# Performance work log

Hardware: AMD Instinct MI355X
Metric: run time of the kernel (lower is better)

The kernel has to match this reference:

```python
import jax, jax.numpy as jnp
import numpy as np

N_HEADS = 16


def _rope(x, cos, sin):
    # x: (B,H,S,hd); cos,sin: (1,1,S,hd//2). Full-dim rotation (rot_dim == head_dim).
    xe = x[..., 0::2]
    xo = x[..., 1::2]
    re = xe * cos - xo * sin
    ro = xe * sin + xo * cos
    return jnp.stack([re, ro], axis=-1).reshape(x.shape)


def setup_inputs() -> dict:
    key = jax.random.key(0)
    B, S, D = 2, 2048, 1024
    hd = D // N_HEADS
    k1, k2, k3, k4, k5 = jax.random.split(key, 5)
    x = jax.random.normal(k1, (B, S, D), dtype=jnp.float32)
    # Linear params (lecun-normal-ish scale)
    w_qkv = jax.random.normal(k2, (D, 3 * D), dtype=jnp.float32) / np.sqrt(D)
    b_qkv = jnp.zeros((3 * D,), dtype=jnp.float32)
    w_out = jax.random.normal(k3, (D, D), dtype=jnp.float32) / np.sqrt(D)
    b_out = jnp.zeros((D,), dtype=jnp.float32)
    # Rotary tables: (S, hd//2)
    inv_freq = 1.0 / (10000.0 ** (np.arange(0, hd, 2, dtype=np.float32) / hd))
    angles = jnp.asarray(np.arange(S, dtype=np.float32)[:, None] * inv_freq[None, :])
    cos = jnp.cos(angles)
    sin = jnp.sin(angles)
    # Causal mask (seq, seq), True = attend
    mask = jnp.tril(jnp.ones((S, S), dtype=bool))
    return {"x": x, "w_qkv": w_qkv, "b_qkv": b_qkv, "w_out": w_out,
            "b_out": b_out, "cos": cos, "sin": sin, "mask": mask}


def reference(x, w_qkv, b_qkv, w_out, b_out, cos, sin, mask):
    B, S, D = x.shape
    H = N_HEADS
    hd = D // H
    scale = hd ** (-0.5)
    qkv = x @ w_qkv + b_qkv  # (B,S,3D)
    qkv = qkv.reshape(B, S, 3, H, hd).transpose(2, 0, 3, 1, 4)  # (3,B,H,S,hd)
    q, k, v = qkv[0], qkv[1], qkv[2]
    c = cos[None, None, :, :]
    s = sin[None, None, :, :]
    q = _rope(q, c, s)
    k = _rope(k, c, s)
    attn = jnp.einsum('bhqd,bhkd->bhqk', q, k) * scale
    attn = jnp.where(mask, attn, -1e9)
    attn = jax.nn.softmax(attn, axis=-1)
    out = jnp.einsum('bhqk,bhkd->bhqd', attn, v)
    out = out.transpose(0, 2, 1, 3).reshape(B, S, D)
    return out @ w_out + b_out
```

## Files before the change

kernel.cpp:

```cpp
#include <hip/hip_runtime.h>
#include <stdint.h>

typedef unsigned short u16;
typedef __attribute__((ext_vector_type(8))) __bf16 bf16x8;
typedef __attribute__((ext_vector_type(4))) float f32x4;
typedef __attribute__((ext_vector_type(4))) unsigned short u16x4;

__device__ __forceinline__ float bf2f(u16 u){
  unsigned int x = ((unsigned int)u) << 16;
  return __builtin_bit_cast(float, x);
}
__device__ __forceinline__ u16 f2bf(float f){
  return __builtin_bit_cast(u16, (__bf16)f);
}
__device__ __forceinline__ float fexp2(float x){ return __builtin_exp2f(x); }
__device__ __forceinline__ void lds_load16(const void* g, void* l){
  __builtin_amdgcn_global_load_lds(
      (const __attribute__((address_space(1))) unsigned int*)g,
      (__attribute__((address_space(3))) unsigned int*)l, 16, 0, 0);
}

__global__ __launch_bounds__(256) void transpose64(const float* __restrict__ in,
                                                   u16* __restrict__ out,
                                                   int R, int C){
  __shared__ u16 t[64][65];
  const int c0 = blockIdx.x * 64, r0 = blockIdx.y * 64;
  const int tid = threadIdx.x;
  const int rr = tid >> 3;
  const int cc = (tid & 7) * 8;
#pragma unroll
  for (int i = 0; i < 2; i++){
    int r = i * 32 + rr;
    const float* p = in + (size_t)(r0 + r) * C + c0 + cc;
    f32x4 v0 = *(const f32x4*)p;
    f32x4 v1 = *(const f32x4*)(p + 4);
#pragma unroll
    for (int j = 0; j < 4; j++){ t[r][cc + j] = f2bf(v0[j]); t[r][cc + 4 + j] = f2bf(v1[j]); }
  }
  __syncthreads();
#pragma unroll
  for (int i = 0; i < 2; i++){
    int c = i * 32 + rr;
    u16 tmp[8];
#pragma unroll
    for (int j = 0; j < 8; j++) tmp[j] = t[cc + j][c];
    *(bf16x8*)(out + (size_t)(c0 + c) * R + r0 + cc) = *(const bf16x8*)tmp;
  }
}

__global__ __launch_bounds__(256) void convert_bf16(const float* __restrict__ in,
                                                    u16* __restrict__ out){
  int t = blockIdx.x * 256 + threadIdx.x;
  const float* p = in + (size_t)t * 8;
  f32x4 v0 = *(const f32x4*)p;
  f32x4 v1 = *(const f32x4*)(p + 4);
  u16 tmp[8];
#pragma unroll
  for (int j = 0; j < 4; j++){ tmp[j] = f2bf(v0[j]); tmp[4 + j] = f2bf(v1[j]); }
  *(bf16x8*)(out + (size_t)t * 8) = *(const bf16x8*)tmp;
}

__global__ __launch_bounds__(256) void v_transpose(const u16* __restrict__ qkv,
                                                   u16* __restrict__ vT){
  const int S = 2048, LD = 3072;
  __shared__ u16 t[64][65];
  const int bh = blockIdx.y;
  const int b = bh >> 4, h = bh & 15;
  const int s0 = blockIdx.x * 64;
  const u16* src = qkv + (size_t)b * S * LD + 2048 + h * 64;
  const int tid = threadIdx.x;
  const int rr = tid >> 3;
  const int cc = (tid & 7) * 8;
#pragma unroll
  for (int i = 0; i < 2; i++){
    int s = i * 32 + rr;
    bf16x8 v = *(const bf16x8*)(src + (size_t)(s0 + s) * LD + cc);
#pragma unroll
    for (int j = 0; j < 8; j++) t[s][cc + j] = __builtin_bit_cast(u16, (__bf16)v[j]);
  }
  __syncthreads();
  u16* dst = vT + (size_t)bh * 64 * S;
#pragma unroll
  for (int i = 0; i < 2; i++){
    int d = i * 32 + rr;
    u16 tmp[8];
#pragma unroll
    for (int j = 0; j < 8; j++) tmp[j] = t[cc + j][d];
    *(bf16x8*)(dst + (size_t)d * S + s0 + cc) = *(const bf16x8*)tmp;
  }
}

template<bool OUTF32, bool ROPE>
__global__ __launch_bounds__(256, 2) void gemm_bt(const u16* __restrict__ A,
                                                  const u16* __restrict__ Bt,
                                                  const float* __restrict__ bias,
                                                  void* __restrict__ Cv,
                                                  int M, int N, int K,
                                                  const float* __restrict__ cosb,
                                                  const float* __restrict__ sinb){
  __shared__ u16 As[128 * 32];
  __shared__ u16 Bs[128 * 32];
  const int nx = gridDim.x;
  const int L = blockIdx.x + nx * blockIdx.y;
  const int per = (nx * gridDim.y) >> 3;
  const int wg = (L & 7) * per + (L >> 3);
  const int bn = wg % nx, bm = wg / nx;
  const int tid = threadIdx.x, w = tid >> 6, l = tid & 63;
  const int lo = l & 15, hi = l >> 4;
  const int wr = (w >> 1) * 64, wc = (w & 1) * 64;
  f32x4 acc[4][4] = {};
  const int lrow = l >> 2, lcd = l & 3;

  for (int k0 = 0; k0 < K; k0 += 32){
#pragma unroll
    for (int i = 0; i < 2; i++){
      int row0 = i * 64 + w * 16;
      int row = row0 + lrow;
      int cs = lcd ^ ((row >> 1) & 3);
      lds_load16(A  + (size_t)(bm * 128 + row) * K + k0 + cs * 8,
                 (char*)As + row0 * 64);
      lds_load16(Bt + (size_t)(bn * 128 + row) * K + k0 + cs * 8,
                 (char*)Bs + row0 * 64);
    }
    __syncthreads();
    bf16x8 a[4], b[4];
#pragma unroll
    for (int mi = 0; mi < 4; mi++){
      int row = wr + mi * 16 + lo;
      unsigned byte = (unsigned)(row * 64 + hi * 16) ^ (((row >> 1) & 3) << 4);
      a[mi] = *(const bf16x8*)((const char*)As + byte);
    }
#pragma unroll
    for (int ni = 0; ni < 4; ni++){
      int row = wc + ni * 16 + lo;
      unsigned byte = (unsigned)(row * 64 + hi * 16) ^ (((row >> 1) & 3) << 4);
      b[ni] = *(const bf16x8*)((const char*)Bs + byte);
    }
    __builtin_amdgcn_s_setprio(1);
#pragma unroll
    for (int mi = 0; mi < 4; mi++)
#pragma unroll
      for (int ni = 0; ni < 4; ni++)
        acc[mi][ni] = __builtin_amdgcn_mfma_f32_16x16x32_bf16(a[mi], b[ni], acc[mi][ni], 0, 0, 0);
    __builtin_amdgcn_s_setprio(0);
    __syncthreads();
  }
  if (ROPE && bn < 16){
#pragma unroll
    for (int mi = 0; mi < 4; mi++){
#pragma unroll
      for (int r = 0; r < 4; r++){
        int grow = bm * 128 + wr + mi * 16 + hi * 4 + r;
        int stok = grow & 2047;
#pragma unroll
        for (int ni = 0; ni < 4; ni++){
          int col = bn * 128 + wc + ni * 16 + lo;
          float v = acc[mi][ni][r] + bias[col];
          float partner = __shfl_xor(v, 1, 64);
          int ip = (col & 63) >> 1;
          float c = cosb[stok * 32 + ip], sn = sinb[stok * 32 + ip];
          float res = (lo & 1) ? (partner * sn + v * c) : (v * c - partner * sn);
          ((u16*)Cv)[(size_t)grow * N + col] = f2bf(res);
        }
      }
    }
  } else {
#pragma unroll
    for (int mi = 0; mi < 4; mi++){
#pragma unroll
      for (int r = 0; r < 4; r++){
        int grow = bm * 128 + wr + mi * 16 + hi * 4 + r;
#pragma unroll
        for (int ni = 0; ni < 4; ni++){
          int col = bn * 128 + wc + ni * 16 + lo;
          float v = acc[mi][ni][r] + bias[col];
          if (OUTF32)
            ((float*)Cv)[(size_t)grow * N + col] = v;
          else
            ((u16*)Cv)[(size_t)grow * N + col] = f2bf(v);
        }
      }
    }
  }
}

#define FA_PHASE(T_, OA_, OB_, MA_, MB_, LA_, LB_)                             \
  {                                                                            \
    const int q0p = (T_) * 32;                                                 \
    const int qrA = q0p + lo, qrB = q0p + 16 + lo;                             \
    const int nkt = (T_) + 1;                                                  \
    const int ch = (nkt + 1) >> 1;                                             \
    const int k0 = w ? ch : 0;                                                 \
    const int k1 = w ? nkt : ch;                                               \
    bf16x8 qfA0, qfA1, qfB0, qfB1;                                             \
    {                                                                          \
      bf16x8 va0 = *(const bf16x8*)(Qp + (size_t)qrA * LD + hi * 8);           \
      bf16x8 va1 = *(const bf16x8*)(Qp + (size_t)qrA * LD + 32 + hi * 8);      \
      bf16x8 vb0 = *(const bf16x8*)(Qp + (size_t)qrB * LD + hi * 8);           \
      bf16x8 vb1 = *(const bf16x8*)(Qp + (size_t)qrB * LD + 32 + hi * 8);      \
      _Pragma("unroll")                                                        \
      for (int j = 0; j < 8; j++){                                             \
        qfA0[j] = (__bf16)((float)va0[j] * QSC);                               \
        qfA1[j] = (__bf16)((float)va1[j] * QSC);                               \
        qfB0[j] = (__bf16)((float)vb0[j] * QSC);                               \
        qfB1[j] = (__bf16)((float)vb1[j] * QSC);                               \
      }                                                                        \
    }                                                                          \
    float lparA = 0.f, lparB = 0.f;                                            \
    MA_ = -1e30f; MB_ = -1e30f;                                                \
    if (k0 < k1){                                                              \
      _Pragma("unroll")                                                        \
      for (int i = 0; i < 4; i++)                                              \
        lds_load16(Kp + (size_t)(k0 * 32 + i * 8 + srow8) * LD + scs * 8,      \
                   (char*)&Ks[w][0][0] + i * 1024);                            \
    }                                                                          \
    int cur = 0;                                                               \
    for (int kt = k0; kt < k1; kt++){                                          \
      bf16x8 vb[4];                                                            \
      _Pragma("unroll")                                                        \
      for (int fd = 0; fd < 4; fd++)                                           \
        vb[fd] = *(const bf16x8*)(Vb + (size_t)(fd * 16 + lo) * S +            \
                                  kt * 32 + hi * 8);                           \
      bf16x8 kb[2][2];                                                         \
      _Pragma("unroll")                                                        \
      for (int c = 0; c < 2; c++){                                             \
        _Pragma("unroll")                                                      \
        for (int f = 0; f < 2; f++){                                           \
          int srw = f * 16 + lo;                                               \
          unsigned byte = ((unsigned)(srw * 128 + c * 64 + hi * 16)) ^         \
                          ((lo & 7) << 4);                                     \
          kb[c][f] = *(const bf16x8*)((const char*)&Ks[w][cur][0] + byte);     \
        }                                                                      \
      }                                                                        \
      if (kt + 1 < k1){                                                        \
        _Pragma("unroll")                                                      \
        for (int i = 0; i < 4; i++)                                            \
          lds_load16(Kp + (size_t)((kt + 1) * 32 + i * 8 + srow8) * LD +       \
                         scs * 8,                                              \
                     (char*)&Ks[w][cur ^ 1][0] + i * 1024);                    \
      }                                                                        \
      f32x4 saA[2] = {}, saB[2] = {};                                          \
      __builtin_amdgcn_s_setprio(1);                                           \
      _Pragma("unroll")                                                        \
      for (int f = 0; f < 2; f++){                                             \
        saA[f] = __builtin_amdgcn_mfma_f32_16x16x32_bf16(kb[0][f], qfA0,       \
                                                         saA[f], 0, 0, 0);     \
        saB[f] = __builtin_amdgcn_mfma_f32_16x16x32_bf16(kb[0][f], qfB0,       \
                                                         saB[f], 0, 0, 0);     \
        saA[f] = __builtin_amdgcn_mfma_f32_16x16x32_bf16(kb[1][f], qfA1,       \
                                                         saA[f], 0, 0, 0);     \
        saB[f] = __builtin_amdgcn_mfma_f32_16x16x32_bf16(kb[1][f], qfB1,       \
                                                         saB[f], 0, 0, 0);     \
      }                                                                        \
      __builtin_amdgcn_s_setprio(0);                                           \
      if (kt == nkt - 1){                                                      \
        _Pragma("unroll")                                                      \
        for (int f = 0; f < 2; f++){                                           \
          int key0 = kt * 32 + f * 16 + hi * 4;                                \
          _Pragma("unroll")                                                    \
          for (int r = 0; r < 4; r++){                                         \
            if (key0 + r > qrA) saA[f][r] = -1e30f;                            \
            if (key0 + r > qrB) saB[f][r] = -1e30f;                            \
          }                                                                    \
        }                                                                      \
      }                                                                        \
      float pmA = fmaxf(                                                       \
          fmaxf(fmaxf(saA[0][0], saA[0][1]), fmaxf(saA[0][2], saA[0][3])),     \
          fmaxf(fmaxf(saA[1][0], saA[1][1]), fmaxf(saA[1][2], saA[1][3])));    \
      float pmB = fmaxf(                                                       \
          fmaxf(fmaxf(saB[0][0], saB[0][1]), fmaxf(saB[0][2], saB[0][3])),     \
          fmaxf(fmaxf(saB[1][0], saB[1][1]), fmaxf(saB[1][2], saB[1][3])));    \
      if (!__all(fmaxf(pmA - MA_, pmB - MB_) <= 11.5f)){                       \
        float rmA = fmaxf(pmA, __shfl_xor(pmA, 16, 64));                       \
        rmA = fmaxf(rmA, __shfl_xor(rmA, 32, 64));                             \
        float rmB = fmaxf(pmB, __shfl_xor(pmB, 16, 64));                       \
        rmB = fmaxf(rmB, __shfl_xor(rmB, 32, 64));                             \
        float mnA = fmaxf(MA_, rmA), mnB = fmaxf(MB_, rmB);                    \
        float cA = fexp2(MA_ - mnA), cB = fexp2(MB_ - mnB);                    \
        MA_ = mnA; MB_ = mnB;                                                  \
        lparA *= cA; lparB *= cB;                                              \
        float cqA[4], cqB[4];                                                  \
        _Pragma("unroll")                                                      \
        for (int r = 0; r < 4; r++){                                           \
          cqA[r] = __shfl(cA, hi * 4 + r, 64);                                 \
          cqB[r] = __shfl(cB, hi * 4 + r, 64);                                 \
        }                                                                      \
        _Pragma("unroll")                                                      \
        for (int fd = 0; fd < 4; fd++){                                        \
          _Pragma("unroll")                                                    \
          for (int r = 0; r < 4; r++){                                         \
            OA_[fd][r] *= cqA[r]; OB_[fd][r] *= cqB[r];                        \
          }                                                                    \
        }                                                                      \
      }                                                                        \
      float pvA[2][4], pvB[2][4];                                              \
      _Pragma("unroll")                                                        \
      for (int f = 0; f < 2; f++){                                             \
        _Pragma("unroll")                                                      \
        for (int r = 0; r < 4; r++){                                           \
          pvA[f][r] = fexp2(saA[f][r] - MA_);                                  \
          pvB[f][r] = fexp2(saB[f][r] - MB_);                                  \
        }                                                                      \
      }                                                                        \
      _Pragma("unroll")                                                        \
      for (int f = 0; f < 2; f++){                                             \
        u16x4 pkA, pkB;                                                        \
        _Pragma("unroll")                                                      \
        for (int r = 0; r < 4; r++){                                           \
          pkA[r] = f2bf(pvA[f][r]); pkB[r] = f2bf(pvB[f][r]);                  \
        }                                                                      \
        *(u16x4*)((char*)&Ps[w][0][0] + lo * 72 + f * 32 + hi * 8) = pkA;      \
        *(u16x4*)((char*)&Ps[w][1][0] + lo * 72 + f * 32 + hi * 8) = pkB;      \
      }                                                                        \
      lparA += ((pvA[0][0] + pvA[0][1]) + (pvA[0][2] + pvA[0][3]))             \
             + ((pvA[1][0] + pvA[1][1]) + (pvA[1][2] + pvA[1][3]));            \
      lparB += ((pvB[0][0] + pvB[0][1]) + (pvB[0][2] + pvB[0][3]))             \
             + ((pvB[1][0] + pvB[1][1]) + (pvB[1][2] + pvB[1][3]));            \
      bf16x8 paA = *(const bf16x8*)((const char*)&Ps[w][0][0] + lo * 72 +      \
                                    hi * 16);                                  \
      bf16x8 paB = *(const bf16x8*)((const char*)&Ps[w][1][0] + lo * 72 +      \
                                    hi * 16);                                  \
      __builtin_amdgcn_s_setprio(1);                                           \
      _Pragma("unroll")                                                        \
      for (int fd = 0; fd < 4; fd++){                                          \
        OA_[fd] = __builtin_amdgcn_mfma_f32_16x16x32_bf16(paA, vb[fd],         \
                                                          OA_[fd], 0, 0, 0);   \
        OB_[fd] = __builtin_amdgcn_mfma_f32_16x16x32_bf16(paB, vb[fd],         \
                                                          OB_[fd], 0, 0, 0);   \
      }                                                                        \
      __builtin_amdgcn_s_setprio(0);                                           \
      cur ^= 1;                                                                \
    }                                                                          \
    lparA += __shfl_xor(lparA, 16, 64); lparA += __shfl_xor(lparA, 32, 64);    \
    lparB += __shfl_xor(lparB, 16, 64); lparB += __shfl_xor(lparB, 32, 64);    \
    LA_ = lparA; LB_ = lparB;                                                  \
  }

#define FA_WRITEPART(slot_, OA_, OB_, MA_, MB_, LA_, LB_)                      \
  {                                                                            \
    _Pragma("unroll")                                                          \
    for (int fd = 0; fd < 4; fd++){                                            \
      u16x4 pkA, pkB;                                                          \
      _Pragma("unroll")                                                        \
      for (int r = 0; r < 4; r++){                                             \
        pkA[r] = f2bf(OA_[fd][r]); pkB[r] = f2bf(OB_[fd][r]);                  \
      }                                                                        \
      *(u16x4*)((char*)&Xo[slot_][0] + (fd * 16 + lo) * 64 + hi * 8) = pkA;    \
      *(u16x4*)((char*)&Xo[slot_][0] + (fd * 16 + lo) * 64 + 32 + hi * 8) = pkB;\
    }                                                                          \
    if (hi == 0){                                                              \
      Xm[slot_][lo] = MA_;      Xl[slot_][lo] = LA_;                           \
      Xm[slot_][16 + lo] = MB_; Xl[slot_][16 + lo] = LB_;                      \
    }                                                                          \
  }

#define FA_COMBINE(slot_, T_, OA_, OB_, MA_, MB_, LA_, LB_)                    \
  {                                                                            \
    const int q0p = (T_) * 32;                                                 \
    u16x4 pA[4], pB[4];                                                        \
    _Pragma("unroll")                                                          \
    for (int fd = 0; fd < 4; fd++){                                            \
      pA[fd] = *(const u16x4*)((const char*)&Xo[slot_][0] +                    \
                               (fd * 16 + lo) * 64 + hi * 8);                  \
      pB[fd] = *(const u16x4*)((const char*)&Xo[slot_][0] +                    \
                               (fd * 16 + lo) * 64 + 32 + hi * 8);             \
    }                                                                          \
    _Pragma("unroll")                                                          \
    for (int r = 0; r < 4; r++){                                               \
      float mOA = __shfl(MA_, hi * 4 + r, 64);                                 \
      float lOA = __shfl(LA_, hi * 4 + r, 64);                                 \
      float mOB = __shfl(MB_, hi * 4 + r, 64);                                 \
      float lOB = __shfl(LB_, hi * 4 + r, 64);                                 \
      float mPA = Xm[slot_][hi * 4 + r], lPA = Xl[slot_][hi * 4 + r];          \
      float mPB = Xm[slot_][16 + hi * 4 + r], lPB = Xl[slot_][16 + hi * 4 + r];\
      float MfA = fmaxf(mOA, mPA), MfB = fmaxf(mOB, mPB);                      \
      float c0A = fexp2(mOA - MfA), c1A = fexp2(mPA - MfA);                    \
      float c0B = fexp2(mOB - MfB), c1B = fexp2(mPB - MfB);                    \
      float invA = 1.0f / (lOA * c0A + lPA * c1A);                             \
      float invB = 1.0f / (lOB * c0B + lPB * c1B);                             \
      int srA = q0p + hi * 4 + r;                                              \
      int srB = q0p + 16 + hi * 4 + r;                                         \
      u16* orA = Oout + (size_t)(b * S + srA) * 1024 + h * 64;                 \
      u16* orB = Oout + (size_t)(b * S + srB) * 1024 + h * 64;                 \
      _Pragma("unroll")                                                        \
      for (int fd = 0; fd < 4; fd++){                                          \
        float vA = (OA_[fd][r] * c0A + bf2f(pA[fd][r]) * c1A) * invA;          \
        float vB = (OB_[fd][r] * c0B + bf2f(pB[fd][r]) * c1B) * invB;          \
        orA[fd * 16 + lo] = f2bf(vA);                                          \
        orB[fd * 16 + lo] = f2bf(vB);                                          \
      }                                                                        \
    }                                                                          \
  }

__global__ __launch_bounds__(128, 2) void flash_attn(const u16* __restrict__ qkv,
                                                     const u16* __restrict__ vT,
                                                     u16* __restrict__ Oout){
  const int S = 2048, LD = 3072;
  const int L = blockIdx.x;
  const int bh = L & 31;
  const int bx = L >> 5;
  const int b = bh >> 4, h = bh & 15;
  const u16* base = qkv + (size_t)b * S * LD;
  const u16* Qp = base + h * 64;
  const u16* Kp = base + 1024 + h * 64;
  const u16* Vb = vT + (size_t)bh * 64 * S;
  const int tid = threadIdx.x, w = tid >> 6, l = tid & 63;
  const int lo = l & 15, hi = l >> 4;
  __shared__ u16 Ks[2][2][32 * 64];
  __shared__ u16 Ps[2][2][16 * 36];
  __shared__ u16 Xo[2][32 * 64];
  __shared__ float Xm[2][32], Xl[2][32];

  const float QSC = 0.125f * 1.44269504089f;
  const int srow8 = l >> 3;
  const int scs = (l & 7) ^ srow8;

  f32x4 o1A[4] = {}, o1B[4] = {};
  f32x4 o2A[4] = {}, o2B[4] = {};
  float m1A, m1B, l1A, l1B, m2A, m2B, l2A, l2B;

  FA_PHASE(63 - bx, o1A, o1B, m1A, m1B, l1A, l1B);
  if (w == 1) FA_WRITEPART(0, o1A, o1B, m1A, m1B, l1A, l1B);
  FA_PHASE(bx,      o2A, o2B, m2A, m2B, l2A, l2B);
  if (w == 0) FA_WRITEPART(1, o2A, o2B, m2A, m2B, l2A, l2B);
  __syncthreads();
  if (w == 0){
    FA_COMBINE(0, 63 - bx, o1A, o1B, m1A, m1B, l1A, l1B);
  } else {
    FA_COMBINE(1, bx,      o2A, o2B, m2A, m2B, l2A, l2B);
  }
}

extern "C" void kernel_launch(void* const* d_in, const int* in_sizes, int n_in,
                              void* d_out, int out_size, void* d_ws, size_t ws_size,
                              hipStream_t stream){
  const float* x     = (const float*)d_in[0];
  const float* w_qkv = (const float*)d_in[1];
  const float* b_qkv = (const float*)d_in[2];
  const float* w_out = (const float*)d_in[3];
  const float* b_out = (const float*)d_in[4];
  const float* cosb  = (const float*)d_in[5];
  const float* sinb  = (const float*)d_in[6];
  float* out = (float*)d_out;
  char* ws = (char*)d_ws;
  u16* qkv  = (u16*)(ws);
  u16* attn = (u16*)(ws + 25165824);
  u16* xbf  = attn;
  u16* wT2  = (u16*)(ws + 33554432);
  u16* wT1  = (u16*)(ws + 35651584);
  u16* vT   = (u16*)(ws + 35651584);

  transpose64<<<dim3(48, 16), 256, 0, stream>>>(w_qkv, wT1, 1024, 3072);
  transpose64<<<dim3(16, 16), 256, 0, stream>>>(w_out, wT2, 1024, 1024);
  convert_bf16<<<2048, 256, 0, stream>>>(x, xbf);
  gemm_bt<false, true ><<<dim3(24, 32), 256, 0, stream>>>(xbf, wT1, b_qkv, qkv,
                                                          4096, 3072, 1024, cosb, sinb);
  v_transpose<<<dim3(32, 32), 256, 0, stream>>>(qkv, vT);
  flash_attn<<<1024, 128, 0, stream>>>(qkv, vT, attn);
  gemm_bt<true , false><<<dim3(8, 32), 256, 0, stream>>>(attn, wT2, b_out, out,
                                                         4096, 1024, 1024, cosb, sinb);
}
```

Before: 129.6 us.

## Merge prep kernels, pad attention combine LDS, raise GEMM occupancy hint

Merges the two weight transposes and the x bf16 conversion into a single prep kernel dispatched by block index, removing two kernel launches and letting the three jobs run concurrently. Pads the flash-attention partial-output LDS rows from 64 to 72 bytes to cut bank conflicts in the cross-wave combine. Raises the GEMM launch-bounds min-blocks hint from 2 to 3, which may force register spills in exchange for higher occupancy.

Measured after the change: 129.3 us. Within noise of the previous version (-0.2%).

```diff
diff --git a/kernel.cpp b/kernel.cpp
--- a/kernel.cpp
+++ b/kernel.cpp
@@ -20,11 +20,11 @@
       (__attribute__((address_space(3))) unsigned int*)l, 16, 0, 0);
 }
 
-__global__ __launch_bounds__(256) void transpose64(const float* __restrict__ in,
-                                                   u16* __restrict__ out,
-                                                   int R, int C){
-  __shared__ u16 t[64][65];
-  const int c0 = blockIdx.x * 64, r0 = blockIdx.y * 64;
+__device__ __forceinline__ void transpose_body(const float* __restrict__ in,
+                                               u16* __restrict__ out,
+                                               int R, int C, int bx, int by,
+                                               u16 (*t)[65]){
+  const int c0 = bx * 64, r0 = by * 64;
   const int tid = threadIdx.x;
   const int rr = tid >> 3;
   const int cc = (tid & 7) * 8;
@@ -48,16 +48,30 @@
   }
 }
 
-__global__ __launch_bounds__(256) void convert_bf16(const float* __restrict__ in,
-                                                    u16* __restrict__ out){
-  int t = blockIdx.x * 256 + threadIdx.x;
-  const float* p = in + (size_t)t * 8;
-  f32x4 v0 = *(const f32x4*)p;
-  f32x4 v1 = *(const f32x4*)(p + 4);
-  u16 tmp[8];
-#pragma unroll
-  for (int j = 0; j < 4; j++){ tmp[j] = f2bf(v0[j]); tmp[4 + j] = f2bf(v1[j]); }
-  *(bf16x8*)(out + (size_t)t * 8) = *(const bf16x8*)tmp;
+__global__ __launch_bounds__(256) void prep(const float* __restrict__ w_qkv,
+                                            const float* __restrict__ w_out,
+                                            const float* __restrict__ x,
+                                            u16* __restrict__ wT1,
+                                            u16* __restrict__ wT2,
+                                            u16* __restrict__ xbf){
+  __shared__ u16 t[64][65];
+  const int bid = blockIdx.x;
+  if (bid < 2048){
+    int i = bid * 256 + threadIdx.x;
+    const float* p = x + (size_t)i * 8;
+    f32x4 v0 = *(const f32x4*)p;
+    f32x4 v1 = *(const f32x4*)(p + 4);
+    u16 tmp[8];
+#pragma unroll
+    for (int j = 0; j < 4; j++){ tmp[j] = f2bf(v0[j]); tmp[4 + j] = f2bf(v1[j]); }
+    *(bf16x8*)(xbf + (size_t)i * 8) = *(const bf16x8*)tmp;
+  } else if (bid < 2048 + 768){
+    int idx = bid - 2048;
+    transpose_body(w_qkv, wT1, 1024, 3072, idx % 48, idx / 48, t);
+  } else {
+    int idx = bid - 2816;
+    transpose_body(w_out, wT2, 1024, 1024, idx % 16, idx / 16, t);
+  }
 }
 
 __global__ __launch_bounds__(256) void v_transpose(const u16* __restrict__ qkv,
@@ -91,7 +105,7 @@
 }
 
 template<bool OUTF32, bool ROPE>
-__global__ __launch_bounds__(256, 2) void gemm_bt(const u16* __restrict__ A,
+__global__ __launch_bounds__(256, 3) void gemm_bt(const u16* __restrict__ A,
                                                   const u16* __restrict__ Bt,
                                                   const float* __restrict__ bias,
                                                   void* __restrict__ Cv,
@@ -345,8 +359,8 @@
       for (int r = 0; r < 4; r++){                                             \
         pkA[r] = f2bf(OA_[fd][r]); pkB[r] = f2bf(OB_[fd][r]);                  \
       }                                                                        \
-      *(u16x4*)((char*)&Xo[slot_][0] + (fd * 16 + lo) * 64 + hi * 8) = pkA;    \
-      *(u16x4*)((char*)&Xo[slot_][0] + (fd * 16 + lo) * 64 + 32 + hi * 8) = pkB;\
+      *(u16x4*)((char*)&Xo[slot_][0] + (fd * 16 + lo) * 72 + hi * 8) = pkA;    \
+      *(u16x4*)((char*)&Xo[slot_][0] + (fd * 16 + lo) * 72 + 32 + hi * 8) = pkB;\
     }                                                                          \
     if (hi == 0){                                                              \
       Xm[slot_][lo] = MA_;      Xl[slot_][lo] = LA_;                           \
@@ -361,9 +375,9 @@
     _Pragma("unroll")                                                          \
     for (int fd = 0; fd < 4; fd++){                                            \
       pA[fd] = *(const u16x4*)((const char*)&Xo[slot_][0] +                    \
-                               (fd * 16 + lo) * 64 + hi * 8);                  \
+                               (fd * 16 + lo) * 72 + hi * 8);                  \
       pB[fd] = *(const u16x4*)((const char*)&Xo[slot_][0] +                    \
-                               (fd * 16 + lo) * 64 + 32 + hi * 8);             \
+                               (fd * 16 + lo) * 72 + 32 + hi * 8);             \
     }                                                                          \
     _Pragma("unroll")                                                          \
     for (int r = 0; r < 4; r++){                                               \
@@ -408,7 +422,7 @@
   const int lo = l & 15, hi = l >> 4;
   __shared__ u16 Ks[2][2][32 * 64];
   __shared__ u16 Ps[2][2][16 * 36];
-  __shared__ u16 Xo[2][32 * 64];
+  __shared__ u16 Xo[2][64 * 36];
   __shared__ float Xm[2][32], Xl[2][32];
 
   const float QSC = 0.125f * 1.44269504089f;
@@ -450,9 +464,7 @@
   u16* wT1  = (u16*)(ws + 35651584);
   u16* vT   = (u16*)(ws + 35651584);
 
-  transpose64<<<dim3(48, 16), 256, 0, stream>>>(w_qkv, wT1, 1024, 3072);
-  transpose64<<<dim3(16, 16), 256, 0, stream>>>(w_out, wT2, 1024, 1024);
-  convert_bf16<<<2048, 256, 0, stream>>>(x, xbf);
+  prep<<<3072, 256, 0, stream>>>(w_qkv, w_out, x, wT1, wT2, xbf);
   gemm_bt<false, true ><<<dim3(24, 32), 256, 0, stream>>>(xbf, wT1, b_qkv, qkv,
                                                           4096, 3072, 1024, cosb, sinb);
   v_transpose<<<dim3(32, 32), 256, 0, stream>>>(qkv, vT);
```
